# Optimization experiments

Hardware: AMD Instinct MI355X
Metric: run time of the kernel (lower is better)

Reference implementation:

```python
import jax, jax.numpy as jnp
import numpy as np

N_NODES = 50000
N_EDGES = 800000
IN_CH, OUT_CH, HEADS = 64, 32, 4
NEG_SLOPE = 0.2
BN_EPS = 1e-5


def setup_inputs() -> dict:
    key = jax.random.key(0)
    ks = jax.random.split(key, 9)
    x = jax.random.normal(ks[0], (N_NODES, IN_CH), dtype=jnp.float32)
    pos = jax.random.uniform(ks[1], (N_NODES, 3), dtype=jnp.float32)
    edge_index = jax.random.randint(ks[2], (2, N_EDGES), 0, N_NODES, dtype=jnp.int64)
    s = 1.0 / np.sqrt(IN_CH)
    W_l = jax.random.normal(ks[3], (IN_CH, HEADS * OUT_CH), dtype=jnp.float32) * s
    W_r = jax.random.normal(ks[4], (IN_CH, HEADS * OUT_CH), dtype=jnp.float32) * s
    W_edge = jax.random.normal(ks[5], (3, HEADS * OUT_CH), dtype=jnp.float32) * 0.5
    att = jax.random.normal(ks[6], (HEADS, OUT_CH), dtype=jnp.float32) * (1.0 / np.sqrt(OUT_CH))
    bn_gamma = jax.random.uniform(ks[7], (HEADS * OUT_CH,), dtype=jnp.float32, minval=0.5, maxval=1.5)
    bn_beta = jax.random.normal(ks[8], (HEADS * OUT_CH,), dtype=jnp.float32) * 0.1
    return {"x": x, "pos": pos, "edge_index": edge_index, "W_l": W_l, "W_r": W_r,
            "W_edge": W_edge, "att": att, "bn_gamma": bn_gamma, "bn_beta": bn_beta}


def reference(x, pos, edge_index, W_l, W_r, W_edge, att, bn_gamma, bn_beta):
    N = x.shape[0]
    H, C = att.shape
    # source->target projections (GATv2: lin_l for source/messages, lin_r for target)
    xl = (x @ W_l).reshape(N, H, C)
    xr = (x @ W_r).reshape(N, H, C)
    src, dst = edge_index[0], edge_index[1]
    edge_attr = pos[src] - pos[dst]  # [E,3] relative position as edge feature
    # add self-loops with fill_value='mean' (PyG default)
    loop = jnp.arange(N)
    src = jnp.concatenate([src, loop])
    dst = jnp.concatenate([dst, loop])
    mean_attr = edge_attr.mean(axis=0, keepdims=True)  # [1,3]
    edge_attr = jnp.concatenate([edge_attr, jnp.broadcast_to(mean_attr, (N, 3))], axis=0)
    # per-edge GATv2 score: att . LeakyReLU(x_l[j] + x_r[i] + W_e e_ij)
    e_feat = (edge_attr @ W_edge).reshape(-1, H, C)
    msg = xl[src]                              # [Et,H,C] (reused for aggregation)
    e = msg + xr[dst] + e_feat
    e = jax.nn.leaky_relu(e, NEG_SLOPE)
    score = jnp.einsum('ehc,hc->eh', e, att)   # [Et,H]
    # segment softmax over destination node
    m = jax.ops.segment_max(score, dst, num_segments=N)
    score = jnp.exp(score - m[dst])
    denom = jax.ops.segment_sum(score, dst, num_segments=N)
    alpha = score / (denom[dst] + 1e-16)       # [Et,H]
    out = jax.ops.segment_sum(alpha[:, :, None] * msg, dst, num_segments=N)
    out = out.reshape(N, H * C)
    # BatchNorm over node dimension (training-mode batch statistics, PyG BatchNorm)
    mu = out.mean(axis=0)
    var = out.var(axis=0)
    return (out - mu) / jnp.sqrt(var + BN_EPS) * bn_gamma + bn_beta
```

## Files before the change

kernel.cpp:

```cpp
#include <hip/hip_runtime.h>
#include <hip/hip_bf16.h>

#define N_NODES 50000
#define IN_CH 64
#define HC 128
#define CAP 64
#define GEMM_BLOCKS (N_NODES / 16)
#define NEG_SLOPE 0.2f
#define BN_EPS 1e-5f


__global__ __launch_bounds__(256) void k_fused(const float* __restrict__ x,
                                               const float* __restrict__ Wl,
                                               const float* __restrict__ Wr,
                                               unsigned int* __restrict__ xl_bf,
                                               float* __restrict__ xr_out,
                                               const int* __restrict__ eidx,
                                               const float* __restrict__ pos,
                                               int* __restrict__ deg,
                                               int* __restrict__ srcs,
                                               float* __restrict__ mean_sums,
                                               int E) {
  __shared__ float xs[16][IN_CH];
  __shared__ __hip_bfloat162 wsm[IN_CH][128];
  __shared__ int s_w64;

  if (blockIdx.x < GEMM_BLOCKS) {
    const int t = threadIdx.x;
    const int row0 = blockIdx.x * 16;

    for (int i = 0; i < 32; ++i) {
      int k = i * 2 + (t >> 7);
      int p = t & 127;
      int cc = p * 2;
      float2 wv;
      if (cc < 128) wv = *(const float2*)(Wl + k * 128 + cc);
      else          wv = *(const float2*)(Wr + k * 128 + (cc - 128));
      wsm[k][p] = __float22bfloat162_rn(wv);
    }
    {
      int r = t >> 4, c4 = (t & 15) * 4;
      *(float4*)&xs[r][c4] = *(const float4*)(x + (row0 + r) * IN_CH + c4);
    }
    __syncthreads();

    const int ct = t & 63;
    const int rt = t >> 6;
    const int c4 = ct * 4;
    const int r4 = rt * 4;

    float acc[4][4];
    #pragma unroll
    for (int a = 0; a < 4; ++a)
      #pragma unroll
      for (int b = 0; b < 4; ++b) acc[a][b] = 0.f;

    #pragma unroll 8
    for (int k = 0; k < IN_CH; ++k) {
      uint2 wraw = *(const uint2*)&wsm[k][ct * 2];
      float2 f01 = __bfloat1622float2(*(__hip_bfloat162*)&wraw.x);
      float2 f23 = __bfloat1622float2(*(__hip_bfloat162*)&wraw.y);
      float wv[4] = {f01.x, f01.y, f23.x, f23.y};
      float xv[4] = {xs[r4][k], xs[r4 + 1][k], xs[r4 + 2][k], xs[r4 + 3][k]};
      #pragma unroll
      for (int a = 0; a < 4; ++a)
        #pragma unroll
        for (int b = 0; b < 4; ++b) acc[a][b] = fmaf(xv[a], wv[b], acc[a][b]);
    }

    #pragma unroll
    for (int a = 0; a < 4; ++a) {
      int row = row0 + r4 + a;
      if (c4 < 128) {
        __hip_bfloat162 b01 = __float22bfloat162_rn(make_float2(acc[a][0], acc[a][1]));
        __hip_bfloat162 b23 = __float22bfloat162_rn(make_float2(acc[a][2], acc[a][3]));
        uint2 u;
        u.x = *(unsigned int*)&b01;
        u.y = *(unsigned int*)&b23;
        *(uint2*)(xl_bf + row * 64 + (c4 >> 1)) = u;
      } else {
        float4 v = make_float4(acc[a][0], acc[a][1], acc[a][2], acc[a][3]);
        *(float4*)(xr_out + row * HC + (c4 - 128)) = v;
      }
    }
    return;
  }

  if (threadIdx.x < 64) {
    int w = eidx[2 * threadIdx.x + 1];
    unsigned long long nz = __ballot(w != 0);
    if (threadIdx.x == 0) s_w64 = (nz == 0ULL) ? 1 : 0;
  }
  __syncthreads();
  const bool w64 = s_w64 != 0;

  const int tid = (blockIdx.x - GEMM_BLOCKS) * 256 + threadIdx.x;
  const int base = tid * 8;
  float sx = 0.f, sy = 0.f, sz = 0.f;

  const bool vec_ok = w64 ? ((E & 1) == 0) : ((E & 3) == 0);

  if (base + 8 <= E && vec_ok) {
    int s[8], d[8];
    if (w64) {
      const int4* ps = (const int4*)(eidx + 2 * base);
      int4 A = ps[0], B = ps[1], C = ps[2], D = ps[3];
      s[0]=A.x; s[1]=A.z; s[2]=B.x; s[3]=B.z; s[4]=C.x; s[5]=C.z; s[6]=D.x; s[7]=D.z;
      const int4* pd = (const int4*)(eidx + 2 * E + 2 * base);
      A = pd[0]; B = pd[1]; C = pd[2]; D = pd[3];
      d[0]=A.x; d[1]=A.z; d[2]=B.x; d[3]=B.z; d[4]=C.x; d[5]=C.z; d[6]=D.x; d[7]=D.z;
    } else {
      int4 A = *(const int4*)(eidx + base);
      int4 B = *(const int4*)(eidx + base + 4);
      s[0]=A.x; s[1]=A.y; s[2]=A.z; s[3]=A.w; s[4]=B.x; s[5]=B.y; s[6]=B.z; s[7]=B.w;
      A = *(const int4*)(eidx + E + base);
      B = *(const int4*)(eidx + E + base + 4);
      d[0]=A.x; d[1]=A.y; d[2]=A.z; d[3]=A.w; d[4]=B.x; d[5]=B.y; d[6]=B.z; d[7]=B.w;
    }
    int slot[8];
    #pragma unroll
    for (int k = 0; k < 8; ++k) slot[k] = atomicAdd(&deg[d[k]], 1);
    #pragma unroll
    for (int k = 0; k < 8; ++k)
      if (slot[k] < CAP - 1) srcs[d[k] * CAP + 1 + slot[k]] = s[k];
    #pragma unroll
    for (int k = 0; k < 8; ++k) {
      sx += pos[3 * s[k]]     - pos[3 * d[k]];
      sy += pos[3 * s[k] + 1] - pos[3 * d[k] + 1];
      sz += pos[3 * s[k] + 2] - pos[3 * d[k] + 2];
    }
  } else if (base < E) {
    int hi = min(base + 8, E);
    for (int e = base; e < hi; ++e) {
      int s, d;
      if (w64) { s = eidx[2 * e]; d = eidx[2 * (E + e)]; }
      else     { s = eidx[e];     d = eidx[E + e]; }
      int o = atomicAdd(&deg[d], 1);
      if (o < CAP - 1) srcs[d * CAP + 1 + o] = s;
      sx += pos[3 * s]     - pos[3 * d];
      sy += pos[3 * s + 1] - pos[3 * d + 1];
      sz += pos[3 * s + 2] - pos[3 * d + 2];
    }
  }

  #pragma unroll
  for (int m = 1; m < 64; m <<= 1) {
    sx += __shfl_xor(sx, m); sy += __shfl_xor(sy, m); sz += __shfl_xor(sz, m);
  }
  float (*red)[3] = (float(*)[3])xs;
  int wave = threadIdx.x >> 6, lane = threadIdx.x & 63;
  if (lane == 0) { red[wave][0] = sx; red[wave][1] = sy; red[wave][2] = sz; }
  __syncthreads();
  if (threadIdx.x == 0) {
    float a = 0.f, b = 0.f, c = 0.f;
    for (int w = 0; w < 4; ++w) { a += red[w][0]; b += red[w][1]; c += red[w][2]; }
    unsafeAtomicAdd(&mean_sums[0], a);
    unsafeAtomicAdd(&mean_sums[1], b);
    unsafeAtomicAdd(&mean_sums[2], c);
  }
}

__device__ __forceinline__ float sum8_dpp(float v) {
  v += __int_as_float(__builtin_amdgcn_mov_dpp(__float_as_int(v), 0xB1,  0xF, 0xF, true));
  v += __int_as_float(__builtin_amdgcn_mov_dpp(__float_as_int(v), 0x4E,  0xF, 0xF, true));
  v += __int_as_float(__builtin_amdgcn_mov_dpp(__float_as_int(v), 0x141, 0xF, 0xF, true));
  return v;
}

__device__ __forceinline__ void edge4(int s, float dx, float dy, float dz, bool valid,
                                      const unsigned int* __restrict__ xl_bf, int l5,
                                      float4 xr4, float4 at4, float4 w0, float4 w1, float4 w2,
                                      float& a0, float& a1, float& a2, float& a3, float& den) {
  uint2 raw = *(const uint2*)(xl_bf + (s << 6) + (l5 << 1));
  float2 x01 = __bfloat1622float2(*(__hip_bfloat162*)&raw.x);
  float2 x23 = __bfloat1622float2(*(__hip_bfloat162*)&raw.y);
  float t0 = x01.x + xr4.x; t0 = fmaf(dx, w0.x, t0); t0 = fmaf(dy, w1.x, t0); t0 = fmaf(dz, w2.x, t0);
  float t1 = x01.y + xr4.y; t1 = fmaf(dx, w0.y, t1); t1 = fmaf(dy, w1.y, t1); t1 = fmaf(dz, w2.y, t1);
  float t2 = x23.x + xr4.z; t2 = fmaf(dx, w0.z, t2); t2 = fmaf(dy, w1.z, t2); t2 = fmaf(dz, w2.z, t2);
  float t3 = x23.y + xr4.w; t3 = fmaf(dx, w0.w, t3); t3 = fmaf(dy, w1.w, t3); t3 = fmaf(dz, w2.w, t3);
  float l0 = fmaxf(t0, NEG_SLOPE * t0);
  float l1 = fmaxf(t1, NEG_SLOPE * t1);
  float l2 = fmaxf(t2, NEG_SLOPE * t2);
  float l3 = fmaxf(t3, NEG_SLOPE * t3);
  float sc = l0 * at4.x;
  sc = fmaf(l1, at4.y, sc); sc = fmaf(l2, at4.z, sc); sc = fmaf(l3, at4.w, sc);
  sc = sum8_dpp(sc);
  float e = __expf(sc);
  float p = valid ? e : 0.f;
  den += p;
  a0 = fmaf(p, x01.x, a0); a1 = fmaf(p, x01.y, a1);
  a2 = fmaf(p, x23.x, a2); a3 = fmaf(p, x23.y, a3);
}

__global__ __launch_bounds__(256) void k_agg(const unsigned int* __restrict__ xl_bf,
                                             float* __restrict__ xr_out,
                                             const float* __restrict__ pos,
                                             const float* __restrict__ att,
                                             const float* __restrict__ We,
                                             const float* __restrict__ mean_sums,
                                             const int* __restrict__ srcs,
                                             const int* __restrict__ deg,
                                             float invE,
                                             float* __restrict__ bn_sums) {
  __shared__ __align__(16) float redS[4][128];
  __shared__ __align__(16) float redQ[4][128];
  const int lane = threadIdx.x & 63;
  const int half = lane >> 5;
  const int l5 = lane & 31;
  const int c = l5 << 2;
  const int wave = threadIdx.x >> 6;

  const float4 at4 = *(const float4*)(att + c);
  const float4 w0 = *(const float4*)(We + c);
  const float4 w1 = *(const float4*)(We + 128 + c);
  const float4 w2 = *(const float4*)(We + 256 + c);
  const float m0 = mean_sums[0] * invE;
  const float m1 = mean_sums[1] * invE;
  const float m2 = mean_sums[2] * invE;

  const int gw = blockIdx.x * 4 + wave;
  const int W = gridDim.x * 4;

  float4 bs = make_float4(0.f, 0.f, 0.f, 0.f);
  float4 bq = make_float4(0.f, 0.f, 0.f, 0.f);

  for (int i = gw; i < N_NODES; i += W) {
    const float4 xr4 = *(const float4*)(xr_out + i * HC + c);
    const float px = pos[3 * i], py = pos[3 * i + 1], pz = pos[3 * i + 2];
    const int di = min(deg[i] + 1, CAP);
    const int sreg = srcs[i * CAP + lane];
    float a0 = 0.f, a1 = 0.f, a2 = 0.f, a3 = 0.f, den = 0.f;

    {
      int sA = __shfl(sreg, 1);
      if (half == 0) sA = i;
      bool vA = half < di;
      if (!vA) sA = i;
      int jB = 2 + half;
      int sB = __shfl(sreg, jB);
      bool vB = jB < di;
      if (!vB) sB = i;
      float pax = pos[3 * sA], pay = pos[3 * sA + 1], paz = pos[3 * sA + 2];
      float pbx = pos[3 * sB], pby = pos[3 * sB + 1], pbz = pos[3 * sB + 2];
      float dxA = (half == 0) ? m0 : pax - px;
      float dyA = (half == 0) ? m1 : pay - py;
      float dzA = (half == 0) ? m2 : paz - pz;
      edge4(sA, dxA, dyA, dzA, vA, xl_bf, l5, xr4, at4, w0, w1, w2, a0, a1, a2, a3, den);
      edge4(sB, pbx - px, pby - py, pbz - pz, vB, xl_bf, l5, xr4, at4, w0, w1, w2, a0, a1, a2, a3, den);
    }

    for (int j = 4; j < di; j += 4) {
      int jA = j + half;
      int jB = j + 2 + half;
      int sA = __shfl(sreg, jA);
      int sB = __shfl(sreg, jB);
      bool vA = jA < di;
      bool vB = jB < di;
      if (!vA) sA = i;
      if (!vB) sB = i;
      float pax = pos[3 * sA], pay = pos[3 * sA + 1], paz = pos[3 * sA + 2];
      float pbx = pos[3 * sB], pby = pos[3 * sB + 1], pbz = pos[3 * sB + 2];
      edge4(sA, pax - px, pay - py, paz - pz, vA, xl_bf, l5, xr4, at4, w0, w1, w2, a0, a1, a2, a3, den);
      edge4(sB, pbx - px, pby - py, pbz - pz, vB, xl_bf, l5, xr4, at4, w0, w1, w2, a0, a1, a2, a3, den);
    }

    den += __shfl_xor(den, 32);
    a0 += __shfl_xor(a0, 32);
    a1 += __shfl_xor(a1, 32);
    a2 += __shfl_xor(a2, 32);
    a3 += __shfl_xor(a3, 32);

    const float inv = 1.f / (den + 1e-16f);
    if (half == 0) {
      float4 o = make_float4(a0 * inv, a1 * inv, a2 * inv, a3 * inv);
      *(float4*)(xr_out + i * HC + c) = o;
      bs.x += o.x; bs.y += o.y; bs.z += o.z; bs.w += o.w;
      bq.x = fmaf(o.x, o.x, bq.x); bq.y = fmaf(o.y, o.y, bq.y);
      bq.z = fmaf(o.z, o.z, bq.z); bq.w = fmaf(o.w, o.w, bq.w);
    }
  }

  if (half == 0) {
    *(float4*)&redS[wave][c] = bs;
    *(float4*)&redQ[wave][c] = bq;
  }
  __syncthreads();
  const int t = threadIdx.x;
  if (t < 128) {
    float s = redS[0][t] + redS[1][t] + redS[2][t] + redS[3][t];
    float q = redQ[0][t] + redQ[1][t] + redQ[2][t] + redQ[3][t];
    unsafeAtomicAdd(&bn_sums[t], s);
    unsafeAtomicAdd(&bn_sums[128 + t], q);
  }
}

__global__ __launch_bounds__(256) void k_bnapply(float* __restrict__ out,
                                                 const float* __restrict__ bn_sums,
                                                 const float* __restrict__ gamma,
                                                 const float* __restrict__ beta,
                                                 int n4) {
  const int stride = gridDim.x * blockDim.x;
  const float invN = 1.f / (float)N_NODES;
  for (int i = blockIdx.x * blockDim.x + threadIdx.x; i < n4; i += stride) {
    int c = (i & 31) * 4;
    float4 v = ((float4*)out)[i];
    float4 s = *(const float4*)(bn_sums + c);
    float4 q = *(const float4*)(bn_sums + 128 + c);
    float4 g = *(const float4*)(gamma + c);
    float4 b = *(const float4*)(beta + c);
    float mu, var, rstd;
    mu = s.x * invN; var = q.x * invN - mu * mu; rstd = rsqrtf(var + BN_EPS);
    v.x = (v.x - mu) * rstd * g.x + b.x;
    mu = s.y * invN; var = q.y * invN - mu * mu; rstd = rsqrtf(var + BN_EPS);
    v.y = (v.y - mu) * rstd * g.y + b.y;
    mu = s.z * invN; var = q.z * invN - mu * mu; rstd = rsqrtf(var + BN_EPS);
    v.z = (v.z - mu) * rstd * g.z + b.z;
    mu = s.w * invN; var = q.w * invN - mu * mu; rstd = rsqrtf(var + BN_EPS);
    v.w = (v.w - mu) * rstd * g.w + b.w;
    ((float4*)out)[i] = v;
  }
}

extern "C" void kernel_launch(void* const* d_in, const int* in_sizes, int n_in,
                              void* d_out, int out_size, void* d_ws, size_t ws_size,
                              hipStream_t stream) {
  const float* x     = (const float*)d_in[0];
  const float* pos   = (const float*)d_in[1];
  const int*   eidx  = (const int*)d_in[2];
  const float* Wl    = (const float*)d_in[3];
  const float* Wr    = (const float*)d_in[4];
  const float* We    = (const float*)d_in[5];
  const float* att   = (const float*)d_in[6];
  const float* gamma = (const float*)d_in[7];
  const float* beta  = (const float*)d_in[8];
  float* out = (float*)d_out;
  const int E = in_sizes[2] / 2;

  char* ws = (char*)d_ws;
  float* mean_sums = (float*)(ws + 64);
  float* bn_sums   = (float*)(ws + 1024);
  int*   deg       = (int*)(ws + 4096);
  int*   srcs      = (int*)(ws + (1 << 19));
  unsigned int* xl_bf = (unsigned int*)(ws + (1 << 24));

  hipMemsetAsync(ws, 0, 4096 + (size_t)N_NODES * 4, stream);

  int eblocks = (E + 2047) / 2048;
  k_fused<<<GEMM_BLOCKS + eblocks, 256, 0, stream>>>(x, Wl, Wr, xl_bf, out,
                                                     eidx, pos, deg, srcs, mean_sums, E);
  k_agg<<<2048, 256, 0, stream>>>(xl_bf, out, pos, att, We, mean_sums, srcs, deg,
                                  1.f / (float)E, bn_sums);
  k_bnapply<<<512, 256, 0, stream>>>(out, bn_sums, gamma, beta, out_size / 4);
}
```

Measured before the change: 257.1 us.

## Split fused GEMM/edge kernel, fold memset into GEMM, use finer edge granularity

The combined GEMM+edge-bucketing kernel is split into two launches. The GEMM kernel now also initialises deg to 1 (self-loop slot), zeroes the reduction buffers and computes the int64-width flag, which removes the separate memset. The edge kernel handles 2 edges per thread instead of 8, giving more parallelism for the atomic scatter. This adds a kernel launch and a serialisation point between GEMM and edge work, which previously ran concurrently in one grid.

```diff
diff --git a/kernel.cpp b/kernel.cpp
--- a/kernel.cpp
+++ b/kernel.cpp
@@ -5,138 +5,140 @@
 #define IN_CH 64
 #define HC 128
 #define CAP 64
-#define GEMM_BLOCKS (N_NODES / 16)
 #define NEG_SLOPE 0.2f
 #define BN_EPS 1e-5f
 
 
-__global__ __launch_bounds__(256) void k_fused(const float* __restrict__ x,
-                                               const float* __restrict__ Wl,
-                                               const float* __restrict__ Wr,
-                                               unsigned int* __restrict__ xl_bf,
-                                               float* __restrict__ xr_out,
-                                               const int* __restrict__ eidx,
+__global__ __launch_bounds__(256) void k_gemm(const float* __restrict__ x,
+                                              const float* __restrict__ Wl,
+                                              const float* __restrict__ Wr,
+                                              unsigned int* __restrict__ xl_bf,
+                                              float* __restrict__ xr_out,
+                                              int* __restrict__ deg,
+                                              float* __restrict__ mean_sums,
+                                              float* __restrict__ bn_sums,
+                                              int* __restrict__ flag,
+                                              const int* __restrict__ eidx) {
+  {
+    int gtid = blockIdx.x * 256 + threadIdx.x;
+    if (gtid < N_NODES) deg[gtid] = 1;
+    if (gtid < 256) bn_sums[gtid] = 0.f;
+    if (gtid < 3) mean_sums[gtid] = 0.f;
+    if (blockIdx.x == 0 && threadIdx.x < 64) {
+      int w = eidx[2 * threadIdx.x + 1];
+      unsigned long long nz = __ballot(w != 0);
+      if (threadIdx.x == 0) flag[0] = (nz == 0ULL) ? 1 : 0;
+    }
+  }
+
+  __shared__ float xs[16][IN_CH];
+  __shared__ __hip_bfloat162 wsm[IN_CH][128];
+  const int t = threadIdx.x;
+  const int row0 = blockIdx.x * 16;
+
+  for (int i = 0; i < 32; ++i) {
+    int k = i * 2 + (t >> 7);
+    int p = t & 127;
+    int cc = p * 2;
+    float2 wv;
+    if (cc < 128) wv = *(const float2*)(Wl + k * 128 + cc);
+    else          wv = *(const float2*)(Wr + k * 128 + (cc - 128));
+    wsm[k][p] = __float22bfloat162_rn(wv);
+  }
+  {
+    int r = t >> 4, c4 = (t & 15) * 4;
+    *(float4*)&xs[r][c4] = *(const float4*)(x + (row0 + r) * IN_CH + c4);
+  }
+  __syncthreads();
+
+  const int ct = t & 63;
+  const int rt = t >> 6;
+  const int c4 = ct * 4;
+  const int r4 = rt * 4;
+
+  float acc[4][4];
+  #pragma unroll
+  for (int a = 0; a < 4; ++a)
+    #pragma unroll
+    for (int b = 0; b < 4; ++b) acc[a][b] = 0.f;
+
+  #pragma unroll 8
+  for (int k = 0; k < IN_CH; ++k) {
+    uint2 wraw = *(const uint2*)&wsm[k][ct * 2];
+    float2 f01 = __bfloat1622float2(*(__hip_bfloat162*)&wraw.x);
+    float2 f23 = __bfloat1622float2(*(__hip_bfloat162*)&wraw.y);
+    float wv[4] = {f01.x, f01.y, f23.x, f23.y};
+    float xv[4] = {xs[r4][k], xs[r4 + 1][k], xs[r4 + 2][k], xs[r4 + 3][k]};
+    #pragma unroll
+    for (int a = 0; a < 4; ++a)
+      #pragma unroll
+      for (int b = 0; b < 4; ++b) acc[a][b] = fmaf(xv[a], wv[b], acc[a][b]);
+  }
+
+  #pragma unroll
+  for (int a = 0; a < 4; ++a) {
+    int row = row0 + r4 + a;
+    if (c4 < 128) {
+      __hip_bfloat162 b01 = __float22bfloat162_rn(make_float2(acc[a][0], acc[a][1]));
+      __hip_bfloat162 b23 = __float22bfloat162_rn(make_float2(acc[a][2], acc[a][3]));
+      uint2 u;
+      u.x = *(unsigned int*)&b01;
+      u.y = *(unsigned int*)&b23;
+      *(uint2*)(xl_bf + row * 64 + (c4 >> 1)) = u;
+    } else {
+      float4 v = make_float4(acc[a][0], acc[a][1], acc[a][2], acc[a][3]);
+      *(float4*)(xr_out + row * HC + (c4 - 128)) = v;
+    }
+  }
+}
+
+__global__ __launch_bounds__(256) void k_edges(const int* __restrict__ eidx,
                                                const float* __restrict__ pos,
                                                int* __restrict__ deg,
                                                int* __restrict__ srcs,
                                                float* __restrict__ mean_sums,
+                                               const int* __restrict__ flag,
                                                int E) {
-  __shared__ float xs[16][IN_CH];
-  __shared__ __hip_bfloat162 wsm[IN_CH][128];
-  __shared__ int s_w64;
-
-  if (blockIdx.x < GEMM_BLOCKS) {
-    const int t = threadIdx.x;
-    const int row0 = blockIdx.x * 16;
-
-    for (int i = 0; i < 32; ++i) {
-      int k = i * 2 + (t >> 7);
-      int p = t & 127;
-      int cc = p * 2;
-      float2 wv;
-      if (cc < 128) wv = *(const float2*)(Wl + k * 128 + cc);
-      else          wv = *(const float2*)(Wr + k * 128 + (cc - 128));
-      wsm[k][p] = __float22bfloat162_rn(wv);
-    }
-    {
-      int r = t >> 4, c4 = (t & 15) * 4;
-      *(float4*)&xs[r][c4] = *(const float4*)(x + (row0 + r) * IN_CH + c4);
-    }
-    __syncthreads();
-
-    const int ct = t & 63;
-    const int rt = t >> 6;
-    const int c4 = ct * 4;
-    const int r4 = rt * 4;
-
-    float acc[4][4];
-    #pragma unroll
-    for (int a = 0; a < 4; ++a)
-      #pragma unroll
-      for (int b = 0; b < 4; ++b) acc[a][b] = 0.f;
-
-    #pragma unroll 8
-    for (int k = 0; k < IN_CH; ++k) {
-      uint2 wraw = *(const uint2*)&wsm[k][ct * 2];
-      float2 f01 = __bfloat1622float2(*(__hip_bfloat162*)&wraw.x);
-      float2 f23 = __bfloat1622float2(*(__hip_bfloat162*)&wraw.y);
-      float wv[4] = {f01.x, f01.y, f23.x, f23.y};
-      float xv[4] = {xs[r4][k], xs[r4 + 1][k], xs[r4 + 2][k], xs[r4 + 3][k]};
-      #pragma unroll
-      for (int a = 0; a < 4; ++a)
-        #pragma unroll
-        for (int b = 0; b < 4; ++b) acc[a][b] = fmaf(xv[a], wv[b], acc[a][b]);
-    }
-
-    #pragma unroll
-    for (int a = 0; a < 4; ++a) {
-      int row = row0 + r4 + a;
-      if (c4 < 128) {
-        __hip_bfloat162 b01 = __float22bfloat162_rn(make_float2(acc[a][0], acc[a][1]));
-        __hip_bfloat162 b23 = __float22bfloat162_rn(make_float2(acc[a][2], acc[a][3]));
-        uint2 u;
-        u.x = *(unsigned int*)&b01;
-        u.y = *(unsigned int*)&b23;
-        *(uint2*)(xl_bf + row * 64 + (c4 >> 1)) = u;
-      } else {
-        float4 v = make_float4(acc[a][0], acc[a][1], acc[a][2], acc[a][3]);
-        *(float4*)(xr_out + row * HC + (c4 - 128)) = v;
-      }
-    }
-    return;
-  }
-
-  if (threadIdx.x < 64) {
-    int w = eidx[2 * threadIdx.x + 1];
-    unsigned long long nz = __ballot(w != 0);
-    if (threadIdx.x == 0) s_w64 = (nz == 0ULL) ? 1 : 0;
-  }
-  __syncthreads();
-  const bool w64 = s_w64 != 0;
-
-  const int tid = (blockIdx.x - GEMM_BLOCKS) * 256 + threadIdx.x;
-  const int base = tid * 8;
+  const bool w64 = flag[0] != 0;
+  const int tid = blockIdx.x * 256 + threadIdx.x;
+  const int base = tid * 2;
   float sx = 0.f, sy = 0.f, sz = 0.f;
 
-  const bool vec_ok = w64 ? ((E & 1) == 0) : ((E & 3) == 0);
-
-  if (base + 8 <= E && vec_ok) {
-    int s[8], d[8];
+  const bool vec_ok = (E & 1) == 0;
+
+  if (base + 2 <= E && vec_ok) {
+    int s[2], d[2];
     if (w64) {
-      const int4* ps = (const int4*)(eidx + 2 * base);
-      int4 A = ps[0], B = ps[1], C = ps[2], D = ps[3];
-      s[0]=A.x; s[1]=A.z; s[2]=B.x; s[3]=B.z; s[4]=C.x; s[5]=C.z; s[6]=D.x; s[7]=D.z;
-      const int4* pd = (const int4*)(eidx + 2 * E + 2 * base);
-      A = pd[0]; B = pd[1]; C = pd[2]; D = pd[3];
-      d[0]=A.x; d[1]=A.z; d[2]=B.x; d[3]=B.z; d[4]=C.x; d[5]=C.z; d[6]=D.x; d[7]=D.z;
+      int4 A = *(const int4*)(eidx + 2 * base);
+      s[0] = A.x; s[1] = A.z;
+      int4 B = *(const int4*)(eidx + 2 * E + 2 * base);
+      d[0] = B.x; d[1] = B.z;
     } else {
-      int4 A = *(const int4*)(eidx + base);
-      int4 B = *(const int4*)(eidx + base + 4);
-      s[0]=A.x; s[1]=A.y; s[2]=A.z; s[3]=A.w; s[4]=B.x; s[5]=B.y; s[6]=B.z; s[7]=B.w;
-      A = *(const int4*)(eidx + E + base);
-      B = *(const int4*)(eidx + E + base + 4);
-      d[0]=A.x; d[1]=A.y; d[2]=A.z; d[3]=A.w; d[4]=B.x; d[5]=B.y; d[6]=B.z; d[7]=B.w;
-    }
-    int slot[8];
-    #pragma unroll
-    for (int k = 0; k < 8; ++k) slot[k] = atomicAdd(&deg[d[k]], 1);
-    #pragma unroll
-    for (int k = 0; k < 8; ++k)
-      if (slot[k] < CAP - 1) srcs[d[k] * CAP + 1 + slot[k]] = s[k];
-    #pragma unroll
-    for (int k = 0; k < 8; ++k) {
+      int2 A = *(const int2*)(eidx + base);
+      s[0] = A.x; s[1] = A.y;
+      int2 B = *(const int2*)(eidx + E + base);
+      d[0] = B.x; d[1] = B.y;
+    }
+    int slot[2];
+    #pragma unroll
+    for (int k = 0; k < 2; ++k) slot[k] = atomicAdd(&deg[d[k]], 1);
+    #pragma unroll
+    for (int k = 0; k < 2; ++k)
+      if (slot[k] < CAP) srcs[d[k] * CAP + slot[k]] = s[k];
+    #pragma unroll
+    for (int k = 0; k < 2; ++k) {
       sx += pos[3 * s[k]]     - pos[3 * d[k]];
       sy += pos[3 * s[k] + 1] - pos[3 * d[k] + 1];
       sz += pos[3 * s[k] + 2] - pos[3 * d[k] + 2];
     }
   } else if (base < E) {
-    int hi = min(base + 8, E);
+    int hi = min(base + 2, E);
     for (int e = base; e < hi; ++e) {
       int s, d;
       if (w64) { s = eidx[2 * e]; d = eidx[2 * (E + e)]; }
       else     { s = eidx[e];     d = eidx[E + e]; }
       int o = atomicAdd(&deg[d], 1);
-      if (o < CAP - 1) srcs[d * CAP + 1 + o] = s;
+      if (o < CAP) srcs[d * CAP + o] = s;
       sx += pos[3 * s]     - pos[3 * d];
       sy += pos[3 * s + 1] - pos[3 * d + 1];
       sz += pos[3 * s + 2] - pos[3 * d + 2];
@@ -147,7 +149,7 @@
   for (int m = 1; m < 64; m <<= 1) {
     sx += __shfl_xor(sx, m); sy += __shfl_xor(sy, m); sz += __shfl_xor(sz, m);
   }
-  float (*red)[3] = (float(*)[3])xs;
+  __shared__ float red[4][3];
   int wave = threadIdx.x >> 6, lane = threadIdx.x & 63;
   if (lane == 0) { red[wave][0] = sx; red[wave][1] = sy; red[wave][2] = sz; }
   __syncthreads();
@@ -227,7 +229,7 @@
   for (int i = gw; i < N_NODES; i += W) {
     const float4 xr4 = *(const float4*)(xr_out + i * HC + c);
     const float px = pos[3 * i], py = pos[3 * i + 1], pz = pos[3 * i + 2];
-    const int di = min(deg[i] + 1, CAP);
+    const int di = min(deg[i], CAP);
     const int sreg = srcs[i * CAP + lane];
     float a0 = 0.f, a1 = 0.f, a2 = 0.f, a3 = 0.f, den = 0.f;
 
@@ -337,17 +339,17 @@
   const int E = in_sizes[2] / 2;
 
   char* ws = (char*)d_ws;
+  int*   flag      = (int*)(ws + 0);
   float* mean_sums = (float*)(ws + 64);
   float* bn_sums   = (float*)(ws + 1024);
   int*   deg       = (int*)(ws + 4096);
   int*   srcs      = (int*)(ws + (1 << 19));
   unsigned int* xl_bf = (unsigned int*)(ws + (1 << 24));
 
-  hipMemsetAsync(ws, 0, 4096 + (size_t)N_NODES * 4, stream);
-
-  int eblocks = (E + 2047) / 2048;
-  k_fused<<<GEMM_BLOCKS + eblocks, 256, 0, stream>>>(x, Wl, Wr, xl_bf, out,
-                                                     eidx, pos, deg, srcs, mean_sums, E);
+  k_gemm<<<N_NODES / 16, 256, 0, stream>>>(x, Wl, Wr, xl_bf, out,
+                                           deg, mean_sums, bn_sums, flag, eidx);
+  int eblocks = (E + 511) / 512;
+  k_edges<<<eblocks, 256, 0, stream>>>(eidx, pos, deg, srcs, mean_sums, flag, E);
   k_agg<<<2048, 256, 0, stream>>>(xl_bf, out, pos, att, We, mean_sums, srcs, deg,
                                   1.f / (float)E, bn_sums);
   k_bnapply<<<512, 256, 0, stream>>>(out, bn_sums, gamma, beta, out_size / 4);
```

After: 288.1 us. 1.12x slower.

## Replace global atomic CSR build with two-pass binned bucketing in shared memory

Applied to the files above, without the earlier changes.

Edges are first binned by destination block of 128 nodes, using per-block shared histograms and one global atomic per bin. A per-bin kernel then builds each node's source list and degree in LDS and writes them out with coalesced stores. This replaces scattered global atomics and scattered srcs writes, and also splits the GEMM out of the fused kernel. The cost is an extra kernel launch and an intermediate binbuf pass, plus fixed capacity limits: BINCAP per bin, and the src/dst packing assumes node ids fit in 16 bits (N=50000 fits) and dl in 8 bits.

```diff
diff --git a/kernel.cpp b/kernel.cpp
--- a/kernel.cpp
+++ b/kernel.cpp
@@ -5,103 +5,39 @@
 #define IN_CH 64
 #define HC 128
 #define CAP 64
-#define GEMM_BLOCKS (N_NODES / 16)
 #define NEG_SLOPE 0.2f
 #define BN_EPS 1e-5f
 
-
-__global__ __launch_bounds__(256) void k_fused(const float* __restrict__ x,
-                                               const float* __restrict__ Wl,
-                                               const float* __restrict__ Wr,
-                                               unsigned int* __restrict__ xl_bf,
-                                               float* __restrict__ xr_out,
-                                               const int* __restrict__ eidx,
-                                               const float* __restrict__ pos,
-                                               int* __restrict__ deg,
-                                               int* __restrict__ srcs,
-                                               float* __restrict__ mean_sums,
-                                               int E) {
-  __shared__ float xs[16][IN_CH];
-  __shared__ __hip_bfloat162 wsm[IN_CH][128];
+#define BIN_SH 7
+#define BIN_N  128
+#define NBINS  391
+#define BINCAP 8192
+
+
+__global__ __launch_bounds__(256) void k_bin(const int* __restrict__ eidx,
+                                             unsigned int* __restrict__ binbuf,
+                                             int* __restrict__ bin_count,
+                                             int E) {
+  __shared__ int hist[NBINS];
+  __shared__ int base_l[NBINS];
   __shared__ int s_w64;
-
-  if (blockIdx.x < GEMM_BLOCKS) {
-    const int t = threadIdx.x;
-    const int row0 = blockIdx.x * 16;
-
-    for (int i = 0; i < 32; ++i) {
-      int k = i * 2 + (t >> 7);
-      int p = t & 127;
-      int cc = p * 2;
-      float2 wv;
-      if (cc < 128) wv = *(const float2*)(Wl + k * 128 + cc);
-      else          wv = *(const float2*)(Wr + k * 128 + (cc - 128));
-      wsm[k][p] = __float22bfloat162_rn(wv);
-    }
-    {
-      int r = t >> 4, c4 = (t & 15) * 4;
-      *(float4*)&xs[r][c4] = *(const float4*)(x + (row0 + r) * IN_CH + c4);
-    }
-    __syncthreads();
-
-    const int ct = t & 63;
-    const int rt = t >> 6;
-    const int c4 = ct * 4;
-    const int r4 = rt * 4;
-
-    float acc[4][4];
-    #pragma unroll
-    for (int a = 0; a < 4; ++a)
-      #pragma unroll
-      for (int b = 0; b < 4; ++b) acc[a][b] = 0.f;
-
-    #pragma unroll 8
-    for (int k = 0; k < IN_CH; ++k) {
-      uint2 wraw = *(const uint2*)&wsm[k][ct * 2];
-      float2 f01 = __bfloat1622float2(*(__hip_bfloat162*)&wraw.x);
-      float2 f23 = __bfloat1622float2(*(__hip_bfloat162*)&wraw.y);
-      float wv[4] = {f01.x, f01.y, f23.x, f23.y};
-      float xv[4] = {xs[r4][k], xs[r4 + 1][k], xs[r4 + 2][k], xs[r4 + 3][k]};
-      #pragma unroll
-      for (int a = 0; a < 4; ++a)
-        #pragma unroll
-        for (int b = 0; b < 4; ++b) acc[a][b] = fmaf(xv[a], wv[b], acc[a][b]);
-    }
-
-    #pragma unroll
-    for (int a = 0; a < 4; ++a) {
-      int row = row0 + r4 + a;
-      if (c4 < 128) {
-        __hip_bfloat162 b01 = __float22bfloat162_rn(make_float2(acc[a][0], acc[a][1]));
-        __hip_bfloat162 b23 = __float22bfloat162_rn(make_float2(acc[a][2], acc[a][3]));
-        uint2 u;
-        u.x = *(unsigned int*)&b01;
-        u.y = *(unsigned int*)&b23;
-        *(uint2*)(xl_bf + row * 64 + (c4 >> 1)) = u;
-      } else {
-        float4 v = make_float4(acc[a][0], acc[a][1], acc[a][2], acc[a][3]);
-        *(float4*)(xr_out + row * HC + (c4 - 128)) = v;
-      }
-    }
-    return;
-  }
 
   if (threadIdx.x < 64) {
     int w = eidx[2 * threadIdx.x + 1];
     unsigned long long nz = __ballot(w != 0);
     if (threadIdx.x == 0) s_w64 = (nz == 0ULL) ? 1 : 0;
   }
+  for (int b = threadIdx.x; b < NBINS; b += 256) hist[b] = 0;
   __syncthreads();
   const bool w64 = s_w64 != 0;
 
-  const int tid = (blockIdx.x - GEMM_BLOCKS) * 256 + threadIdx.x;
+  const int tid = blockIdx.x * 256 + threadIdx.x;
   const int base = tid * 8;
-  float sx = 0.f, sy = 0.f, sz = 0.f;
-
   const bool vec_ok = w64 ? ((E & 1) == 0) : ((E & 3) == 0);
 
+  int s[8], d[8];
+  int n = 0;
   if (base + 8 <= E && vec_ok) {
-    int s[8], d[8];
     if (w64) {
       const int4* ps = (const int4*)(eidx + 2 * base);
       int4 A = ps[0], B = ps[1], C = ps[2], D = ps[3];
@@ -117,37 +53,70 @@
       B = *(const int4*)(eidx + E + base + 4);
       d[0]=A.x; d[1]=A.y; d[2]=A.z; d[3]=A.w; d[4]=B.x; d[5]=B.y; d[6]=B.z; d[7]=B.w;
     }
-    int slot[8];
-    #pragma unroll
-    for (int k = 0; k < 8; ++k) slot[k] = atomicAdd(&deg[d[k]], 1);
-    #pragma unroll
-    for (int k = 0; k < 8; ++k)
-      if (slot[k] < CAP - 1) srcs[d[k] * CAP + 1 + slot[k]] = s[k];
-    #pragma unroll
-    for (int k = 0; k < 8; ++k) {
-      sx += pos[3 * s[k]]     - pos[3 * d[k]];
-      sy += pos[3 * s[k] + 1] - pos[3 * d[k] + 1];
-      sz += pos[3 * s[k] + 2] - pos[3 * d[k] + 2];
-    }
+    n = 8;
   } else if (base < E) {
     int hi = min(base + 8, E);
     for (int e = base; e < hi; ++e) {
-      int s, d;
-      if (w64) { s = eidx[2 * e]; d = eidx[2 * (E + e)]; }
-      else     { s = eidx[e];     d = eidx[E + e]; }
-      int o = atomicAdd(&deg[d], 1);
-      if (o < CAP - 1) srcs[d * CAP + 1 + o] = s;
-      sx += pos[3 * s]     - pos[3 * d];
-      sy += pos[3 * s + 1] - pos[3 * d + 1];
-      sz += pos[3 * s + 2] - pos[3 * d + 2];
-    }
+      if (w64) { s[n] = eidx[2 * e]; d[n] = eidx[2 * (E + e)]; }
+      else     { s[n] = eidx[e];     d[n] = eidx[E + e]; }
+      ++n;
+    }
+  }
+
+  int bin[8], rank[8];
+  for (int k = 0; k < n; ++k) {
+    bin[k] = d[k] >> BIN_SH;
+    rank[k] = atomicAdd(&hist[bin[k]], 1);
+  }
+  __syncthreads();
+  for (int b = threadIdx.x; b < NBINS; b += 256) {
+    int h = hist[b];
+    base_l[b] = h ? atomicAdd(&bin_count[b], h) : 0;
+  }
+  __syncthreads();
+  for (int k = 0; k < n; ++k) {
+    int idx = base_l[bin[k]] + rank[k];
+    if (idx < BINCAP)
+      binbuf[bin[k] * BINCAP + idx] = ((unsigned int)(d[k] & (BIN_N - 1)) << 16) | (unsigned int)s[k];
+  }
+}
+
+__global__ __launch_bounds__(256) void k_bucket(const unsigned int* __restrict__ binbuf,
+                                                const int* __restrict__ bin_count,
+                                                const float* __restrict__ pos,
+                                                int* __restrict__ deg,
+                                                int* __restrict__ srcs,
+                                                float* __restrict__ mean_sums) {
+  __shared__ unsigned int srcs_l[BIN_N * CAP];
+  __shared__ int deg_l[BIN_N];
+  __shared__ float red[4][3];
+
+  const int bin = blockIdx.x;
+  const int nbase = bin << BIN_SH;
+  const int nn = min(BIN_N, N_NODES - nbase);
+
+  if (threadIdx.x < BIN_N) deg_l[threadIdx.x] = 1;
+  __syncthreads();
+
+  const int cnt = min(bin_count[bin], BINCAP);
+  float sx = 0.f, sy = 0.f, sz = 0.f;
+
+  for (int t = threadIdx.x; t < cnt; t += 256) {
+    unsigned int rec = binbuf[bin * BINCAP + t];
+    int s  = (int)(rec & 0xffffu);
+    int dl = (int)((rec >> 16) & 0xffu);
+    int slot = atomicAdd(&deg_l[dl], 1);
+    if (slot < CAP) srcs_l[(dl << 6) + slot] = (unsigned int)s;
+    int dg = nbase + dl;
+    sx += pos[3 * s]     - pos[3 * dg];
+    sy += pos[3 * s + 1] - pos[3 * dg + 1];
+    sz += pos[3 * s + 2] - pos[3 * dg + 2];
   }
 
   #pragma unroll
   for (int m = 1; m < 64; m <<= 1) {
     sx += __shfl_xor(sx, m); sy += __shfl_xor(sy, m); sz += __shfl_xor(sz, m);
   }
-  float (*red)[3] = (float(*)[3])xs;
   int wave = threadIdx.x >> 6, lane = threadIdx.x & 63;
   if (lane == 0) { red[wave][0] = sx; red[wave][1] = sy; red[wave][2] = sz; }
   __syncthreads();
@@ -157,6 +126,78 @@
     unsafeAtomicAdd(&mean_sums[0], a);
     unsafeAtomicAdd(&mean_sums[1], b);
     unsafeAtomicAdd(&mean_sums[2], c);
+  }
+
+  if (threadIdx.x < nn) deg[nbase + threadIdx.x] = deg_l[threadIdx.x];
+  const int nw4 = nn << 4;
+  uint4* dstp = (uint4*)(srcs + (size_t)nbase * CAP);
+  const uint4* srcp = (const uint4*)srcs_l;
+  for (int t = threadIdx.x; t < nw4; t += 256) dstp[t] = srcp[t];
+}
+
+__global__ __launch_bounds__(256) void k_gemm(const float* __restrict__ x,
+                                              const float* __restrict__ Wl,
+                                              const float* __restrict__ Wr,
+                                              unsigned int* __restrict__ xl_bf,
+                                              float* __restrict__ xr_out) {
+  __shared__ float xs[16][IN_CH];
+  __shared__ __hip_bfloat162 wsm[IN_CH][128];
+  const int t = threadIdx.x;
+  const int row0 = blockIdx.x * 16;
+
+  for (int i = 0; i < 32; ++i) {
+    int k = i * 2 + (t >> 7);
+    int p = t & 127;
+    int cc = p * 2;
+    float2 wv;
+    if (cc < 128) wv = *(const float2*)(Wl + k * 128 + cc);
+    else          wv = *(const float2*)(Wr + k * 128 + (cc - 128));
+    wsm[k][p] = __float22bfloat162_rn(wv);
+  }
+  {
+    int r = t >> 4, c4 = (t & 15) * 4;
+    *(float4*)&xs[r][c4] = *(const float4*)(x + (row0 + r) * IN_CH + c4);
+  }
+  __syncthreads();
+
+  const int ct = t & 63;
+  const int rt = t >> 6;
+  const int c4 = ct * 4;
+  const int r4 = rt * 4;
+
+  float acc[4][4];
+  #pragma unroll
+  for (int a = 0; a < 4; ++a)
+    #pragma unroll
+    for (int b = 0; b < 4; ++b) acc[a][b] = 0.f;
+
+  #pragma unroll 8
+  for (int k = 0; k < IN_CH; ++k) {
+    uint2 wraw = *(const uint2*)&wsm[k][ct * 2];
+    float2 f01 = __bfloat1622float2(*(__hip_bfloat162*)&wraw.x);
+    float2 f23 = __bfloat1622float2(*(__hip_bfloat162*)&wraw.y);
+    float wv[4] = {f01.x, f01.y, f23.x, f23.y};
+    float xv[4] = {xs[r4][k], xs[r4 + 1][k], xs[r4 + 2][k], xs[r4 + 3][k]};
+    #pragma unroll
+    for (int a = 0; a < 4; ++a)
+      #pragma unroll
+      for (int b = 0; b < 4; ++b) acc[a][b] = fmaf(xv[a], wv[b], acc[a][b]);
+  }
+
+  #pragma unroll
+  for (int a = 0; a < 4; ++a) {
+    int row = row0 + r4 + a;
+    if (c4 < 128) {
+      __hip_bfloat162 b01 = __float22bfloat162_rn(make_float2(acc[a][0], acc[a][1]));
+      __hip_bfloat162 b23 = __float22bfloat162_rn(make_float2(acc[a][2], acc[a][3]));
+      uint2 u;
+      u.x = *(unsigned int*)&b01;
+      u.y = *(unsigned int*)&b23;
+      *(uint2*)(xl_bf + row * 64 + (c4 >> 1)) = u;
+    } else {
+      float4 v = make_float4(acc[a][0], acc[a][1], acc[a][2], acc[a][3]);
+      *(float4*)(xr_out + row * HC + (c4 - 128)) = v;
+    }
   }
 }
 
@@ -227,7 +268,7 @@
   for (int i = gw; i < N_NODES; i += W) {
     const float4 xr4 = *(const float4*)(xr_out + i * HC + c);
     const float px = pos[3 * i], py = pos[3 * i + 1], pz = pos[3 * i + 2];
-    const int di = min(deg[i] + 1, CAP);
+    const int di = min(deg[i], CAP);
     const int sreg = srcs[i * CAP + lane];
     float a0 = 0.f, a1 = 0.f, a2 = 0.f, a3 = 0.f, den = 0.f;
 
@@ -337,17 +378,20 @@
   const int E = in_sizes[2] / 2;
 
   char* ws = (char*)d_ws;
-  float* mean_sums = (float*)(ws + 64);
-  float* bn_sums   = (float*)(ws + 1024);
-  int*   deg       = (int*)(ws + 4096);
-  int*   srcs      = (int*)(ws + (1 << 19));
-  unsigned int* xl_bf = (unsigned int*)(ws + (1 << 24));
-
-  hipMemsetAsync(ws, 0, 4096 + (size_t)N_NODES * 4, stream);
-
-  int eblocks = (E + 2047) / 2048;
-  k_fused<<<GEMM_BLOCKS + eblocks, 256, 0, stream>>>(x, Wl, Wr, xl_bf, out,
-                                                     eidx, pos, deg, srcs, mean_sums, E);
+  float* mean_sums     = (float*)(ws + 64);
+  float* bn_sums       = (float*)(ws + 1024);
+  int*   bin_count     = (int*)(ws + 4096);
+  int*   deg           = (int*)(ws + 8192);
+  int*   srcs          = (int*)(ws + 208896);
+  unsigned int* binbuf = (unsigned int*)(ws + 13008896);
+  unsigned int* xl_bf  = (unsigned int*)(ws + 25821184);
+
+  hipMemsetAsync(ws, 0, 8192, stream);
+
+  int bblocks = (E + 2047) / 2048;
+  k_bin<<<bblocks, 256, 0, stream>>>(eidx, binbuf, bin_count, E);
+  k_bucket<<<NBINS, 256, 0, stream>>>(binbuf, bin_count, pos, deg, srcs, mean_sums);
+  k_gemm<<<N_NODES / 16, 256, 0, stream>>>(x, Wl, Wr, xl_bf, out);
   k_agg<<<2048, 256, 0, stream>>>(xl_bf, out, pos, att, We, mean_sums, srcs, deg,
                                   1.f / (float)E, bn_sums);
   k_bnapply<<<512, 256, 0, stream>>>(out, bn_sums, gamma, beta, out_size / 4);
```

Result: faster. 239.5 us (median of 2 runs) (-6.8%).
